# Optimization experiments

Hardware: AMD Instinct MI355X
Metric: run time of the kernel (lower is better)

## Reference

```python
import jax, jax.numpy as jnp
import numpy as np


def _lstm_cell(x, h, c, Wih, Whh, b):
    # torch LSTM gate order: i, f, g, o
    g = x @ Wih.T + h @ Whh.T + b
    i, f, gg, o = jnp.split(g, 4, axis=-1)
    c = jax.nn.sigmoid(f) * c + jax.nn.sigmoid(i) * jnp.tanh(gg)
    h = jax.nn.sigmoid(o) * jnp.tanh(c)
    return h, c


def _run_lstm(emb, mask, Wih, Whh, b, reverse):
    # mask-gated scan emulates pack_padded_sequence: state frozen on pad steps,
    # final (h, c) equals state at last valid token of each sequence.
    B = emb.shape[0]
    H = Whh.shape[1]
    def step(carry, inp):
        h, c = carry
        x, m = inp  # x: (B, E), m: (B, 1)
        hn, cn = _lstm_cell(x, h, c, Wih, Whh, b)
        h = m * hn + (1.0 - m) * h
        c = m * cn + (1.0 - m) * c
        return (h, c), h
    xs = (jnp.swapaxes(emb, 0, 1), jnp.swapaxes(mask, 0, 1)[..., None])
    z = jnp.zeros((B, H), emb.dtype)
    (h, c), outs = jax.lax.scan(step, (z, z), xs, reverse=reverse)
    return jnp.swapaxes(outs, 0, 1), h, c  # (B, T, H), (B, H), (B, H)


def setup_inputs() -> dict:
    key = jax.random.key(0)
    ks = iter(jax.random.split(key, 40))
    B, Te, Td, E, H, Ve, Vd = 32, 64, 32, 256, 512, 32000, 32000
    s = 0.05
    def rn(shape):
        return jax.random.normal(next(ks), shape, jnp.float32) * s
    def zz(n):
        return jnp.zeros((n,), jnp.float32)
    return {
        "enc_texts": jax.random.randint(next(ks), (B, Te), 0, Ve),
        "enc_mask": jnp.ones((B, Te), jnp.float32),
        "dec_texts": jax.random.randint(next(ks), (B, Td), 0, Vd),
        "enc_emb": rn((Ve, E)),
        "dec_emb": rn((Vd, E)),
        "Wih_f": rn((4 * H, E)), "Whh_f": rn((4 * H, H)), "b_f": zz(4 * H),
        "Wih_b": rn((4 * H, E)), "Whh_b": rn((4 * H, H)), "b_b": zz(4 * H),
        "Wih_d": rn((4 * H, E + 2 * H)), "Whh_d": rn((4 * H, H)), "b_d": zz(4 * H),
        "W_h": rn((H, 2 * H)), "b_h": zz(H),
        "W_c": rn((H, 2 * H)), "b_c": zz(H),
        "W_df": rn((2 * H, 2 * H)), "b_df": zz(2 * H),
        "W_ef": rn((2 * H, 2 * H)), "b_ef": zz(2 * H),
        "W_out": rn((Vd, 3 * H)), "b_out": zz(Vd),
    }


def reference(enc_texts, enc_mask, dec_texts, enc_emb, dec_emb,
              Wih_f, Whh_f, b_f, Wih_b, Whh_b, b_b,
              Wih_d, Whh_d, b_d, W_h, b_h, W_c, b_c,
              W_df, b_df, W_ef, b_ef, W_out, b_out):
    B = enc_texts.shape[0]
    H = Whh_d.shape[1]
    # ---- encode: bidirectional LSTM over embedded source ----
    emb = enc_emb[enc_texts]  # (B, Te, E)
    out_f, hf, cf = _run_lstm(emb, enc_mask, Wih_f, Whh_f, b_f, reverse=False)
    out_b, hb, cb = _run_lstm(emb, enc_mask, Wih_b, Whh_b, b_b, reverse=True)
    enc_output = jnp.concatenate([out_f, out_b], -1) * enc_mask[..., None]  # (B, Te, 2H)
    # ---- decode_init: project concat of directional final states ----
    dec_h = jax.nn.relu(jnp.concatenate([hf, hb], -1) @ W_h.T + b_h)  # (B, H)
    dec_c = jax.nn.relu(jnp.concatenate([cf, cb], -1) @ W_c.T + b_c)  # (B, H)
    # precompute attention keys once (enc_output_fc)
    enc_feat = enc_output @ W_ef.T + b_ef  # (B, Te, 2H)
    # teacher-forcing inputs: tokens 0..Td-2
    dec_in = dec_emb[dec_texts[:, :-1]]  # (B, Td-1, E)
    ctx0 = jnp.zeros((B, 2 * H), enc_output.dtype)

    def step(carry, x):
        h, c, ctx = carry
        xin = jnp.concatenate([x, ctx], -1)  # (B, E + 2H)
        h, c = _lstm_cell(xin, h, c, Wih_d, Whh_d, b_d)
        # dot attention: query from projected (h, c)
        df = jnp.concatenate([h, c], -1) @ W_df.T + b_df  # (B, 2H)
        scores = jnp.einsum('bd,btd->bt', df, enc_feat)
        a = jax.nn.softmax(scores, axis=-1) * enc_mask
        a = a / jnp.sum(a, axis=-1, keepdims=True)
        ctx = jnp.einsum('bt,btd->bd', a, enc_output)  # (B, 2H)
        logits = jnp.concatenate([h, ctx], -1) @ W_out.T + b_out  # (B, Vd)
        return (h, c, ctx), logits

    _, logits = jax.lax.scan(step, (dec_h, dec_c, ctx0), jnp.swapaxes(dec_in, 0, 1))
    return jnp.swapaxes(logits, 0, 1)  # (B, Td-1, Vd)
```

## Files before the change

### kernel.cpp

```cpp
#include <hip/hip_runtime.h>
#include <hip/hip_bf16.h>


typedef __attribute__((ext_vector_type(8))) short bfrag_t;
typedef __attribute__((ext_vector_type(4))) float f4_t;

static __device__ __forceinline__ float bf2f(unsigned short u) {
  union { float f; unsigned int i; } v; v.i = ((unsigned int)u) << 16; return v.f;
}
static __device__ __forceinline__ unsigned short f2bf(float f) {
  union { float f; unsigned int i; } v; v.f = f;
  unsigned int r = v.i + 0x7FFFu + ((v.i >> 16) & 1u);
  return (unsigned short)(r >> 16);
}
static __device__ __forceinline__ unsigned int pack_bf2(float lo, float hi) {
  __hip_bfloat162 h2 = __float22bfloat162_rn(make_float2(lo, hi));
  union { __hip_bfloat162 h; unsigned int u; } cv; cv.h = h2;
  return cv.u;
}
static __device__ __forceinline__ float sigm(float x) {
  return __builtin_amdgcn_rcpf(1.f + __expf(-x));
}
static __device__ __forceinline__ float ftanh(float x) {
  float e = __expf(2.f * x);
  return 1.f - 2.f * __builtin_amdgcn_rcpf(e + 1.f);
}

#define GLDS16(g, l)                                                        \
  __builtin_amdgcn_global_load_lds(                                         \
      (const __attribute__((address_space(1))) void*)(g),                   \
      (__attribute__((address_space(3))) void*)(l), 16, 0, 0)

static __device__ __forceinline__ void st_f32_coh(float* p, float v) {
  asm volatile("global_store_dword %0, %1, off sc0 sc1" :: "v"(p), "v"(v) : "memory");
}
static __device__ __forceinline__ void st_u16_coh(unsigned short* p, unsigned short x) {
  asm volatile("global_store_short %0, %1, off sc0 sc1" :: "v"(p), "v"((unsigned)x) : "memory");
}
static __device__ __forceinline__ float ld_f32_coh(const float* p) {
  float v;
  asm volatile("global_load_dword %0, %1, off sc0 sc1\n\ts_waitcnt vmcnt(0)"
               : "=v"(v) : "v"(p) : "memory");
  return v;
}

static __device__ __forceinline__ void gbar8(unsigned* base, unsigned target) {
  __syncthreads();
  if (threadIdx.x < 64) {
    if (threadIdx.x == 0)
      __hip_atomic_fetch_add(base + (blockIdx.x & 7) * 32, 1u,
                             __ATOMIC_RELAXED, __HIP_MEMORY_SCOPE_AGENT);
    unsigned sum;
    do {
      unsigned v = 0;
      if (threadIdx.x < 8)
        v = __hip_atomic_load(base + threadIdx.x * 32,
                              __ATOMIC_RELAXED, __HIP_MEMORY_SCOPE_AGENT);
      v += __shfl_xor(v, 1);
      v += __shfl_xor(v, 2);
      v += __shfl_xor(v, 4);
      sum = __shfl(v, 0);
      if (sum < target) __builtin_amdgcn_s_sleep(2);
    } while (sum < target);
  }
  __syncthreads();
}

__global__ __launch_bounds__(256) void gemm_bt_kernel(
    const unsigned short* __restrict__ A, int lda,
    const float* __restrict__ B, int ldb, int bcol0,
    const float* __restrict__ bias, void* __restrict__ Cv, int ldc,
    int Mvalid, int K, int Mt, int swz, int obf) {
  __shared__ unsigned short As[128 * 32];
  __shared__ unsigned short Bs[128 * 32];
  int id = blockIdx.x;
  if (swz) { int x = id & 7; id = x * ((int)gridDim.x >> 3) + (id >> 3); }
  const int mb = id % Mt, nb = id / Mt;
  const int m0 = mb * 128, n0 = nb * 128;
  const int tid = threadIdx.x;
  const int w = tid >> 6, lane = tid & 63;
  const int wr = (w >> 1) * 64, wc = (w & 1) * 64;
  const int l15 = lane & 15, l4 = lane >> 4;

  const int arow = w * 16 + (lane >> 2);
  const int acol = (lane & 3) * 8;
  const unsigned short* Ag = A + (size_t)(m0 + arow) * lda + acol;

  const int brow = tid >> 1;
  const int bcol = (tid & 1) * 16;
  const float* Bg = B + (size_t)(n0 + brow) * ldb + bcol0 + bcol;
  unsigned short* Bsw = Bs + brow * 32 + bcol;

  f4_t acc[4][4];
#pragma unroll
  for (int i = 0; i < 4; ++i)
#pragma unroll
    for (int j = 0; j < 4; ++j) {
      acc[i][j].x = 0.f; acc[i][j].y = 0.f; acc[i][j].z = 0.f; acc[i][j].w = 0.f;
    }

  for (int kt = 0; kt < K; kt += 32) {
    GLDS16(Ag + kt, As + w * 512);
    GLDS16(Ag + (size_t)64 * lda + kt, As + (4 + w) * 512);
    float4 q0 = *(const float4*)(Bg + kt);
    float4 q1 = *(const float4*)(Bg + kt + 4);
    float4 q2 = *(const float4*)(Bg + kt + 8);
    float4 q3 = *(const float4*)(Bg + kt + 12);
    union { unsigned int u[8]; uint4 q[2]; } pk;
    pk.u[0] = pack_bf2(q0.x, q0.y); pk.u[1] = pack_bf2(q0.z, q0.w);
    pk.u[2] = pack_bf2(q1.x, q1.y); pk.u[3] = pack_bf2(q1.z, q1.w);
    pk.u[4] = pack_bf2(q2.x, q2.y); pk.u[5] = pack_bf2(q2.z, q2.w);
    pk.u[6] = pack_bf2(q3.x, q3.y); pk.u[7] = pack_bf2(q3.z, q3.w);
    *(uint4*)(Bsw) = pk.q[0];
    *(uint4*)(Bsw + 8) = pk.q[1];
    __syncthreads();
    bfrag_t af[4], bfv[4];
#pragma unroll
    for (int m = 0; m < 4; ++m)
      af[m] = *(const bfrag_t*)(As + (wr + m * 16 + l15) * 32 + l4 * 8);
#pragma unroll
    for (int n = 0; n < 4; ++n)
      bfv[n] = *(const bfrag_t*)(Bs + (wc + n * 16 + l15) * 32 + l4 * 8);
#pragma unroll
    for (int m = 0; m < 4; ++m)
#pragma unroll
      for (int n = 0; n < 4; ++n)
        acc[m][n] = __builtin_amdgcn_mfma_f32_16x16x32_bf16(af[m], bfv[n], acc[m][n], 0, 0, 0);
    __syncthreads();
  }

  const int crb = l4 * 4;
  float* Cf = (float*)Cv;
  unsigned short* Ch = (unsigned short*)Cv;
#pragma unroll
  for (int m = 0; m < 4; ++m)
#pragma unroll
    for (int n = 0; n < 4; ++n)
#pragma unroll
      for (int r = 0; r < 4; ++r) {
        int gr = m0 + wr + m * 16 + crb + r;
        if (gr < Mvalid) {
          int gc = n0 + wc + n * 16 + l15;
          float v = acc[m][n][r] + (bias ? bias[gc] : 0.f);
          if (obf) Ch[(size_t)gr * ldc + gc] = f2bf(v);
          else     Cf[(size_t)gr * ldc + gc] = v;
        }
      }
}

__global__ void gather_enc_kernel(const int* __restrict__ texts,
                                  const float* __restrict__ table,
                                  unsigned short* __restrict__ out) {
  const int row = blockIdx.x;
  const int tok = texts[row];
  const float4 v = *(const float4*)(table + (size_t)tok * 256 + threadIdx.x * 4);
  unsigned short* o = out + (size_t)row * 256 + threadIdx.x * 4;
  o[0] = f2bf(v.x); o[1] = f2bf(v.y); o[2] = f2bf(v.z); o[3] = f2bf(v.w);
}

__global__ void gather_dec_kernel(const int* __restrict__ texts,
                                  const float* __restrict__ table,
                                  unsigned short* __restrict__ out) {
  const int row = blockIdx.x;
  unsigned short* o = out + (size_t)row * 256 + threadIdx.x * 4;
  if (row >= 992) { o[0] = 0; o[1] = 0; o[2] = 0; o[3] = 0; return; }
  const int b = row / 31, t2 = row - b * 31;
  const int tok = texts[b * 32 + t2];
  const float4 v = *(const float4*)(table + (size_t)tok * 256 + threadIdx.x * 4);
  o[0] = f2bf(v.x); o[1] = f2bf(v.y); o[2] = f2bf(v.z); o[3] = f2bf(v.w);
}

__global__ __launch_bounds__(256) void wdf_t_kernel(
    const float* __restrict__ W_df, const float* __restrict__ b_df,
    float* __restrict__ WT) {
  const int bid = blockIdx.x;
  if (bid < 1024) {
    __shared__ float tl[32][33];
    const int tx = (bid & 31) * 32, ty = (bid >> 5) * 32;
    const int r = threadIdx.x >> 5, c = threadIdx.x & 31;
#pragma unroll
    for (int i = 0; i < 4; ++i)
      tl[r + i * 8][c] = W_df[(size_t)(ty + r + i * 8) * 1024 + tx + c];
    __syncthreads();
#pragma unroll
    for (int i = 0; i < 4; ++i)
      WT[(size_t)(tx + r + i * 8) * 1024 + ty + c] = tl[c][r + i * 8];
  } else {
    for (int i = threadIdx.x; i < 1024; i += 256)
      WT[(size_t)1024 * 1024 + i] = b_df[i];
  }
}

__global__ __launch_bounds__(256) void mega_enc_kernel(
    const float* __restrict__ XF, const float* __restrict__ XB,
    const float* __restrict__ Whh_f, const float* __restrict__ Whh_b,
    const float* __restrict__ mask,
    unsigned short* __restrict__ HBF,
    unsigned short* __restrict__ ENCO, float* __restrict__ HFIN,
    unsigned* bar) {
  const int bi = blockIdx.x;
  const int dir = bi >> 7;
  const int u0 = (bi & 127) * 4;
  const int tid = threadIdx.x;
  const float* X = dir ? XB : XF;
  const float* W = dir ? Whh_b : Whh_f;
  unsigned short* Hbf = HBF + dir * 32768;
  unsigned* cnt = bar + dir * 256;

  __shared__ unsigned short WA[16 * 520];
  __shared__ unsigned short HB[32 * 520];
  __shared__ float Gl[16][33];

#pragma unroll
  for (int i = 0; i < 8; ++i) {
    int idx = tid + i * 256;
    int r = idx >> 7, c4 = idx & 127;
    const float4 v = *(const float4*)(W + (size_t)((r >> 2) * 512 + u0 + (r & 3)) * 512 + c4 * 4);
    *(uint2*)(WA + r * 520 + c4 * 4) = make_uint2(pack_bf2(v.x, v.y), pack_bf2(v.z, v.w));
  }
  __syncthreads();

  const int w = tid >> 6, lane = tid & 63;
  const int l15 = lane & 15, l4 = lane >> 4;

  bfrag_t afr[16];
  if (w < 2) {
#pragma unroll
    for (int kk = 0; kk < 16; ++kk)
      afr[kk] = *(const bfrag_t*)(WA + l15 * 520 + kk * 32 + l4 * 8);
  }

  const int ob = tid & 31, ouo = (tid >> 5) & 3;
  const int ou = u0 + ouo;
  float h_reg = 0.f, c_reg = 0.f;

  unsigned tgt = 0;
  for (int s = 0; s < 64; ++s) {
    const int t = dir ? (63 - s) : s;
    const int pp = s & 1;
    float xg0 = 0, xg1 = 0, xg2 = 0, xg3 = 0, mval = 0;
    if (tid < 128) {
      const float* xp = X + ((size_t)ob * 64 + t) * 2048 + ou;
      xg0 = xp[0]; xg1 = xp[512]; xg2 = xp[1024]; xg3 = xp[1536];
      mval = mask[ob * 64 + t];
    }
    const unsigned short* hsrc = Hbf + pp * 16384;
    uint4 tmp[8];
#pragma unroll
    for (int i = 0; i < 8; ++i) {
      int idx = tid + i * 256;
      int r = idx >> 6, c = idx & 63;
      asm volatile("global_load_dwordx4 %0, %1, off sc0 sc1"
                   : "=v"(tmp[i]) : "v"(hsrc + r * 512 + c * 8));
    }
    asm volatile("s_waitcnt vmcnt(0)" ::: "memory");
#pragma unroll
    for (int i = 0; i < 8; ++i) {
      int idx = tid + i * 256;
      int r = idx >> 6, c = idx & 63;
      *(uint4*)(HB + r * 520 + c * 8) = tmp[i];
    }
    __syncthreads();
    if (w < 2) {
      f4_t ae = {0.f, 0.f, 0.f, 0.f}, ao = {0.f, 0.f, 0.f, 0.f};
#pragma unroll
      for (int kk = 0; kk < 16; kk += 2) {
        bfrag_t b0 = *(const bfrag_t*)(HB + (w * 16 + l15) * 520 + kk * 32 + l4 * 8);
        bfrag_t b1 = *(const bfrag_t*)(HB + (w * 16 + l15) * 520 + (kk + 1) * 32 + l4 * 8);
        ae = __builtin_amdgcn_mfma_f32_16x16x32_bf16(afr[kk], b0, ae, 0, 0, 0);
        ao = __builtin_amdgcn_mfma_f32_16x16x32_bf16(afr[kk + 1], b1, ao, 0, 0, 0);
      }
#pragma unroll
      for (int r = 0; r < 4; ++r)
        Gl[l4 * 4 + r][w * 16 + l15] = ae[r] + ao[r];
    }
    __syncthreads();
    if (tid < 128) {
      float gi = Gl[ouo][ob] + xg0;
      float gf = Gl[4 + ouo][ob] + xg1;
      float gg = Gl[8 + ouo][ob] + xg2;
      float go = Gl[12 + ouo][ob] + xg3;
      float cn = sigm(gf) * c_reg + sigm(gi) * ftanh(gg);
      float hn = sigm(go) * ftanh(cn);
      float hmix = mval * hn + (1.f - mval) * h_reg;
      float cmix = mval * cn + (1.f - mval) * c_reg;
      h_reg = hmix; c_reg = cmix;
      ENCO[((size_t)ob * 64 + t) * 1024 + dir * 512 + ou] = f2bf(hmix * mval);
      st_u16_coh(Hbf + (pp ^ 1) * 16384 + ob * 512 + ou, f2bf(hmix));
      if (s == 63) {
        HFIN[dir * 16384 + ob * 512 + ou] = hmix;
        HFIN[(2 + dir) * 16384 + ob * 512 + ou] = cmix;
      }
    }
    if (s < 63) { tgt += 128; gbar8(cnt, tgt); }
  }
}

__global__ __launch_bounds__(256) void mega_dec_kernel(
    const float* __restrict__ HFIN, const float* __restrict__ W_h,
    const float* __restrict__ b_h, const float* __restrict__ W_c,
    const float* __restrict__ b_c, const float* __restrict__ XD,
    const float* __restrict__ Wih_d, const float* __restrict__ Whh_d,
    const unsigned short* __restrict__ EFG, const unsigned short* __restrict__ ENCO,
    const float* __restrict__ mask, float* __restrict__ DECH,
    float* __restrict__ DECC, unsigned short* __restrict__ PRE0,
    unsigned short* __restrict__ ACAT, unsigned* bar) {
  const int bi = blockIdx.x;
  const int tid = threadIdx.x;
  const bool is_attn = (bi >= 128);
  const int u0 = bi * 4;

  __shared__ union {
    struct {
      unsigned short wga[16 * 1544];
      unsigned short xb[32 * 1544];
      float gl[16][33];
    } s;
    struct {
      unsigned short efg[64 * 1160];
      float hcl[1024];
      float scl[64];
      float al[64];
    } a;
    struct { float xl[32][132]; float wi[8][132]; } ini;
  } U;

  if (!is_attn) {
    const int mat = bi >> 6, j0i = (bi & 63) * 8;
    const int jj = tid >> 5, b = tid & 31;
    const int sr = tid >> 5, sc = (tid & 31) * 4;
    const float* Wm = mat ? W_c : W_h;
    const float* bias = mat ? b_c : b_h;
    const float* x0 = HFIN + (size_t)(mat ? 2 : 0) * 16384;
    const float* x1 = HFIN + (size_t)(mat ? 3 : 1) * 16384;
    float acc = 0.f;
    for (int kc = 0; kc < 1024; kc += 128) {
#pragma unroll
      for (int i = 0; i < 4; ++i) {
        int r = sr + i * 8;
        const float* src = (kc < 512) ? (x0 + r * 512 + kc + sc)
                                      : (x1 + r * 512 + (kc - 512) + sc);
        *(float4*)&U.ini.xl[r][sc] = *(const float4*)src;
      }
      *(float4*)&U.ini.wi[sr][sc] = *(const float4*)(Wm + (size_t)(j0i + sr) * 1024 + kc + sc);
      __syncthreads();
#pragma unroll
      for (int k = 0; k < 128; k += 4) {
        float4 wv = *(const float4*)&U.ini.wi[jj][k];
        float4 xv = *(const float4*)&U.ini.xl[b][k];
        acc += wv.x * xv.x + wv.y * xv.y + wv.z * xv.z + wv.w * xv.w;
      }
      __syncthreads();
    }
    float v = fmaxf(acc + bias[j0i + jj], 0.f);
    if (mat == 0) {
      st_f32_coh(DECH + b * 512 + j0i + jj, v);
      st_u16_coh(PRE0 + (size_t)b * 1536 + j0i + jj, f2bf(v));
    } else {
      st_f32_coh(DECC + b * 512 + j0i + jj, v);
    }
  } else {
    const int b = bi - 128;
    for (int idx = tid; idx < 64 * 144; idx += 256) {
      int s = idx / 144, c16 = idx - (idx / 144) * 144;
      *(uint4*)(U.a.efg + s * 1160 + c16 * 8) =
          *(const uint4*)(EFG + ((size_t)b * 64 + s) * 1152 + c16 * 8);
    }
  }
  unsigned tgt = 160;
  gbar8(bar, tgt);

  const int ob = tid & 31, ouo = (tid >> 5) & 3, ou = u0 + ouo;
  const int w = tid >> 6, lane = tid & 63;
  const int l15 = lane & 15, l4 = lane >> 4;
  float h_reg = 0.f, c_reg = 0.f;

  if (!is_attn) {
#pragma unroll
    for (int i = 0; i < 24; ++i) {
      int idx = tid + i * 256;
      int r = idx / 384, c4 = idx - (idx / 384) * 384;
      int wrow = (r >> 2) * 512 + u0 + (r & 3);
      int c = c4 * 4;
      float4 v;
      if (c < 512) v = *(const float4*)(Whh_d + (size_t)wrow * 512 + c);
      else         v = *(const float4*)(Wih_d + (size_t)wrow * 1280 + 256 + (c - 512));
      *(uint2*)(U.s.wga + r * 1544 + c) = make_uint2(pack_bf2(v.x, v.y), pack_bf2(v.z, v.w));
    }
    if (tid < 128) {
      h_reg = ld_f32_coh(DECH + ob * 512 + ou);
      c_reg = ld_f32_coh(DECC + ob * 512 + ou);
    }
  }

  for (int t = 0; t < 31; ++t) {
    if (!is_attn) {
      float xg0 = 0, xg1 = 0, xg2 = 0, xg3 = 0;
      if (tid < 128) {
        const float* xp = XD + ((size_t)ob * 31 + t) * 2048 + ou;
        xg0 = xp[0]; xg1 = xp[512]; xg2 = xp[1024]; xg3 = xp[1536];
      }
      {
        uint4 tmp[24];
#pragma unroll
        for (int i = 0; i < 24; ++i) {
          int idx = tid + i * 256;
          int r = idx / 192, c16 = idx - (idx / 192) * 192;
          const unsigned short* src = (t == 0)
              ? (PRE0 + (size_t)r * 1536 + c16 * 8)
              : (ACAT + ((size_t)r * 31 + (t - 1)) * 1536 + c16 * 8);
          asm volatile("global_load_dwordx4 %0, %1, off sc0 sc1"
                       : "=v"(tmp[i]) : "v"(src));
        }
        asm volatile("s_waitcnt vmcnt(16)" ::: "memory");
#pragma unroll
        for (int i = 0; i < 8; ++i) {
          int idx = tid + i * 256;
          int r = idx / 192, c16 = idx - (idx / 192) * 192;
          *(uint4*)(U.s.xb + r * 1544 + c16 * 8) = tmp[i];
        }
        asm volatile("s_waitcnt vmcnt(8)" ::: "memory");
#pragma unroll
        for (int i = 8; i < 16; ++i) {
          int idx = tid + i * 256;
          int r = idx / 192, c16 = idx - (idx / 192) * 192;
          *(uint4*)(U.s.xb + r * 1544 + c16 * 8) = tmp[i];
        }
        asm volatile("s_waitcnt vmcnt(0)" ::: "memory");
#pragma unroll
        for (int i = 16; i < 24; ++i) {
          int idx = tid + i * 256;
          int r = idx / 192, c16 = idx - (idx / 192) * 192;
          *(uint4*)(U.s.xb + r * 1544 + c16 * 8) = tmp[i];
        }
      }
      __syncthreads();
      if (w < 2) {
        f4_t ae = {0.f, 0.f, 0.f, 0.f}, ao = {0.f, 0.f, 0.f, 0.f};
#pragma unroll
        for (int kk = 0; kk < 48; kk += 2) {
          bfrag_t a0 = *(const bfrag_t*)(U.s.wga + l15 * 1544 + kk * 32 + l4 * 8);
          bfrag_t b0 = *(const bfrag_t*)(U.s.xb + (w * 16 + l15) * 1544 + kk * 32 + l4 * 8);
          bfrag_t a1 = *(const bfrag_t*)(U.s.wga + l15 * 1544 + (kk + 1) * 32 + l4 * 8);
          bfrag_t b1 = *(const bfrag_t*)(U.s.xb + (w * 16 + l15) * 1544 + (kk + 1) * 32 + l4 * 8);
          ae = __builtin_amdgcn_mfma_f32_16x16x32_bf16(a0, b0, ae, 0, 0, 0);
          ao = __builtin_amdgcn_mfma_f32_16x16x32_bf16(a1, b1, ao, 0, 0, 0);
        }
#pragma unroll
        for (int r = 0; r < 4; ++r)
          U.s.gl[l4 * 4 + r][w * 16 + l15] = ae[r] + ao[r];
      }
      __syncthreads();
      if (tid < 128) {
        float gi = U.s.gl[ouo][ob] + xg0;
        float gf = U.s.gl[4 + ouo][ob] + xg1;
        float gg = U.s.gl[8 + ouo][ob] + xg2;
        float go = U.s.gl[12 + ouo][ob] + xg3;
        float cn = sigm(gf) * c_reg + sigm(gi) * ftanh(gg);
        float hn = sigm(go) * ftanh(cn);
        h_reg = hn; c_reg = cn;
        st_f32_coh(DECH + ob * 512 + ou, hn);
        st_f32_coh(DECC + ob * 512 + ou, cn);
        st_u16_coh(ACAT + ((size_t)ob * 31 + t) * 1536 + ou, f2bf(hn));
      }
    }
    tgt += 160;
    gbar8(bar, tgt);
    if (is_attn) {
      const int b = bi - 128;
      {
        int c = tid * 4;
        const float* hp = (c < 512) ? (DECH + b * 512 + c) : (DECC + b * 512 + (c - 512));
        uint4 hv;
        asm volatile("global_load_dwordx4 %0, %1, off sc0 sc1\n\ts_waitcnt vmcnt(0)"
                     : "=v"(hv) : "v"(hp) : "memory");
        *(uint4*)&U.a.hcl[c] = hv;
      }
      __syncthreads();
      {
        const int sidx = tid >> 2, part = tid & 3;
        const unsigned short* eg = U.a.efg + sidx * 1160 + part * 256;
        const float* d = &U.a.hcl[part * 256];
        float acc = 0.f;
#pragma unroll 8
        for (int k = 0; k < 256; k += 8) {
          uint4 v = *(const uint4*)(eg + k);
          acc += bf2f((unsigned short)(v.x & 0xFFFFu)) * d[k + 0];
          acc += bf2f((unsigned short)(v.x >> 16))     * d[k + 1];
          acc += bf2f((unsigned short)(v.y & 0xFFFFu)) * d[k + 2];
          acc += bf2f((unsigned short)(v.y >> 16))     * d[k + 3];
          acc += bf2f((unsigned short)(v.z & 0xFFFFu)) * d[k + 4];
          acc += bf2f((unsigned short)(v.z >> 16))     * d[k + 5];
          acc += bf2f((unsigned short)(v.w & 0xFFFFu)) * d[k + 6];
          acc += bf2f((unsigned short)(v.w >> 16))     * d[k + 7];
        }
        acc += __shfl_xor(acc, 1);
        acc += __shfl_xor(acc, 2);
        if (part == 0)
          U.a.scl[sidx] = acc + bf2f(U.a.efg[sidx * 1160 + 1024]);
      }
      __syncthreads();
      if (tid < 64) {
        float v = U.a.scl[tid];
        float mx = v;
#pragma unroll
        for (int o = 32; o >= 1; o >>= 1) mx = fmaxf(mx, __shfl_xor(mx, o));
        float e = __expf(v - mx) * mask[b * 64 + tid];
        float sm = e;
#pragma unroll
        for (int o = 32; o >= 1; o >>= 1) sm += __shfl_xor(sm, o);
        U.a.al[tid] = e / sm;
      }
      __syncthreads();
      float c0 = 0.f, c1 = 0.f, c2 = 0.f, c3 = 0.f;
#pragma unroll 8
      for (int tp = 0; tp < 64; ++tp) {
        float a = U.a.al[tp];
        const unsigned short* eo = ENCO + ((size_t)b * 64 + tp) * 1024 + tid;
        c0 += a * bf2f(eo[0]);
        c1 += a * bf2f(eo[256]);
        c2 += a * bf2f(eo[512]);
        c3 += a * bf2f(eo[768]);
      }
      unsigned short* ap = ACAT + ((size_t)b * 31 + t) * 1536 + 512;
      st_u16_coh(ap + tid, f2bf(c0));
      st_u16_coh(ap + tid + 256, f2bf(c1));
      st_u16_coh(ap + tid + 512, f2bf(c2));
      st_u16_coh(ap + tid + 768, f2bf(c3));
    }
    if (t < 30) { tgt += 160; gbar8(bar, tgt); }
  }
}

extern "C" void kernel_launch(void* const* d_in, const int* in_sizes, int n_in,
                              void* d_out, int out_size, void* d_ws, size_t ws_size,
                              hipStream_t stream) {
  const int*   enc_texts = (const int*)  d_in[0];
  const float* enc_mask  = (const float*)d_in[1];
  const int*   dec_texts = (const int*)  d_in[2];
  const float* enc_emb   = (const float*)d_in[3];
  const float* dec_emb   = (const float*)d_in[4];
  const float* Wih_f = (const float*)d_in[5];
  const float* Whh_f = (const float*)d_in[6];
  const float* b_f   = (const float*)d_in[7];
  const float* Wih_b = (const float*)d_in[8];
  const float* Whh_b = (const float*)d_in[9];
  const float* b_b   = (const float*)d_in[10];
  const float* Wih_d = (const float*)d_in[11];
  const float* Whh_d = (const float*)d_in[12];
  const float* b_d   = (const float*)d_in[13];
  const float* W_h   = (const float*)d_in[14];
  const float* b_h   = (const float*)d_in[15];
  const float* W_c   = (const float*)d_in[16];
  const float* b_c   = (const float*)d_in[17];
  const float* W_df  = (const float*)d_in[18];
  const float* b_df  = (const float*)d_in[19];
  const float* W_ef  = (const float*)d_in[20];
  const float* b_ef  = (const float*)d_in[21];
  const float* W_out = (const float*)d_in[22];
  const float* b_out = (const float*)d_in[23];
  float* out = (float*)d_out;

  char* ws = (char*)d_ws;
  size_t off = 0;
  auto alloc = [&](size_t bytes) {
    char* p = ws + off;
    off += (bytes + 255) & ~(size_t)255;
    return p;
  };
  unsigned short* HBF  = (unsigned short*)alloc((size_t)2 * 2 * 16384 * 2);
  float* DECH = (float*)alloc((size_t)16384 * 4);
  float* DECC = (float*)alloc((size_t)16384 * 4);
  unsigned short* PRE0 = (unsigned short*)alloc((size_t)32 * 1536 * 2);
  unsigned short* ACAT = (unsigned short*)alloc((size_t)1024 * 1536 * 2);
  unsigned* bar = (unsigned*)alloc(4096);
  size_t zbytes = off;
  float* XF = (float*)alloc((size_t)2048 * 2048 * 4);
  float* XB = (float*)alloc((size_t)2048 * 2048 * 4);
  float* XD = (float*)alloc((size_t)1024 * 2048 * 4);
  unsigned short* EFb  = (unsigned short*)alloc((size_t)2048 * 1024 * 2);
  unsigned short* ENCO = (unsigned short*)alloc((size_t)2048 * 1024 * 2);
  unsigned short* EMBB = (unsigned short*)alloc((size_t)2048 * 256 * 2);
  unsigned short* DEMB = (unsigned short*)alloc((size_t)1024 * 256 * 2);
  float* HFIN = (float*)alloc((size_t)4 * 16384 * 4);
  unsigned short* EFG = (unsigned short*)XF;
  float* WT  = XB;

  hipMemsetAsync(d_ws, 0, zbytes, stream);

  gather_enc_kernel<<<2048, 64, 0, stream>>>(enc_texts, enc_emb, EMBB);
  gather_dec_kernel<<<1024, 64, 0, stream>>>(dec_texts, dec_emb, DEMB);

  dim3 blk(256);
  gemm_bt_kernel<<<256, blk, 0, stream>>>(EMBB, 256, Wih_f, 256, 0, b_f, XF, 2048, 2048, 256, 16, 0, 0);
  gemm_bt_kernel<<<256, blk, 0, stream>>>(EMBB, 256, Wih_b, 256, 0, b_b, XB, 2048, 2048, 256, 16, 0, 0);
  gemm_bt_kernel<<<128, blk, 0, stream>>>(DEMB, 256, Wih_d, 1280, 0, b_d, XD, 2048, 1024, 256, 8, 0, 0);

  mega_enc_kernel<<<256, blk, 0, stream>>>(XF, XB, Whh_f, Whh_b, enc_mask, HBF, ENCO, HFIN, bar);

  wdf_t_kernel<<<1025, blk, 0, stream>>>(W_df, b_df, WT);
  gemm_bt_kernel<<<128, blk, 0, stream>>>(ENCO, 1024, W_ef, 1024, 0, b_ef, EFb, 1024, 2048, 1024, 16, 0, 1);
  gemm_bt_kernel<<<144, blk, 0, stream>>>(EFb, 1024, WT, 1024, 0, nullptr, EFG, 1152, 2048, 1024, 16, 0, 1);

  mega_dec_kernel<<<160, blk, 0, stream>>>(HFIN, W_h, b_h, W_c, b_c, XD, Wih_d, Whh_d,
                                           EFG, ENCO, enc_mask, DECH, DECC, PRE0, ACAT, bar + 512);

  gemm_bt_kernel<<<2000, blk, 0, stream>>>(ACAT, 1536, W_out, 1536, 0, b_out, out, 32000, 992, 1536, 8, 1, 0);
}
```

Baseline: 1.346 ms.

## Halve encoder blocks and split decoder barrier into two overlapped phases

The encoder recurrence now uses 128 blocks that each own 8 hidden units, with all four waves doing MFMA work. This halves the number of blocks taking part in each per-step grid barrier. In the decoder, the single 160-block barrier becomes two split arrive/wait barriers, one between LSTM blocks and one from attention blocks to LSTM blocks. The LSTM blocks precompute the h-part of the next step's gate GEMM while the attention context is still being computed, which shortens the serial critical path per step. The cost is more complex synchronization, with a risk of ordering or coherence bugs, and higher per-block work and register use in the encoder.

```diff
diff --git a/kernel.cpp b/kernel.cpp
--- a/kernel.cpp
+++ b/kernel.cpp
@@ -44,12 +44,14 @@
   return v;
 }
 
-static __device__ __forceinline__ void gbar8(unsigned* base, unsigned target) {
+static __device__ __forceinline__ void arrive8(unsigned* base) {
   __syncthreads();
+  if (threadIdx.x == 0)
+    __hip_atomic_fetch_add(base + (blockIdx.x & 7) * 32, 1u,
+                           __ATOMIC_RELAXED, __HIP_MEMORY_SCOPE_AGENT);
+}
+static __device__ __forceinline__ void wait8(unsigned* base, unsigned target) {
   if (threadIdx.x < 64) {
-    if (threadIdx.x == 0)
-      __hip_atomic_fetch_add(base + (blockIdx.x & 7) * 32, 1u,
-                             __ATOMIC_RELAXED, __HIP_MEMORY_SCOPE_AGENT);
     unsigned sum;
     do {
       unsigned v = 0;
@@ -64,6 +66,10 @@
     } while (sum < target);
   }
   __syncthreads();
+}
+static __device__ __forceinline__ void gbar8(unsigned* base, unsigned target) {
+  arrive8(base);
+  wait8(base, target);
 }
 
 __global__ __launch_bounds__(256) void gemm_bt_kernel(
@@ -199,38 +205,37 @@
     unsigned short* __restrict__ ENCO, float* __restrict__ HFIN,
     unsigned* bar) {
   const int bi = blockIdx.x;
-  const int dir = bi >> 7;
-  const int u0 = (bi & 127) * 4;
+  const int dir = bi >> 6;
+  const int u0 = (bi & 63) * 8;
   const int tid = threadIdx.x;
   const float* X = dir ? XB : XF;
   const float* W = dir ? Whh_b : Whh_f;
   unsigned short* Hbf = HBF + dir * 32768;
   unsigned* cnt = bar + dir * 256;
 
-  __shared__ unsigned short WA[16 * 520];
+  __shared__ unsigned short WA[32 * 520];
   __shared__ unsigned short HB[32 * 520];
-  __shared__ float Gl[16][33];
-
-#pragma unroll
-  for (int i = 0; i < 8; ++i) {
+  __shared__ float Gl[32][33];
+
+#pragma unroll
+  for (int i = 0; i < 16; ++i) {
     int idx = tid + i * 256;
     int r = idx >> 7, c4 = idx & 127;
-    const float4 v = *(const float4*)(W + (size_t)((r >> 2) * 512 + u0 + (r & 3)) * 512 + c4 * 4);
+    const float4 v = *(const float4*)(W + (size_t)((r >> 3) * 512 + u0 + (r & 7)) * 512 + c4 * 4);
     *(uint2*)(WA + r * 520 + c4 * 4) = make_uint2(pack_bf2(v.x, v.y), pack_bf2(v.z, v.w));
   }
   __syncthreads();
 
   const int w = tid >> 6, lane = tid & 63;
   const int l15 = lane & 15, l4 = lane >> 4;
+  const int wrow = (w >> 1) * 16, wcol = (w & 1) * 16;
 
   bfrag_t afr[16];
-  if (w < 2) {
-#pragma unroll
-    for (int kk = 0; kk < 16; ++kk)
-      afr[kk] = *(const bfrag_t*)(WA + l15 * 520 + kk * 32 + l4 * 8);
-  }
-
-  const int ob = tid & 31, ouo = (tid >> 5) & 3;
+#pragma unroll
+  for (int kk = 0; kk < 16; ++kk)
+    afr[kk] = *(const bfrag_t*)(WA + (wrow + l15) * 520 + kk * 32 + l4 * 8);
+
+  const int ob = tid & 31, ouo = tid >> 5;
   const int ou = u0 + ouo;
   float h_reg = 0.f, c_reg = 0.f;
 
@@ -238,12 +243,9 @@
   for (int s = 0; s < 64; ++s) {
     const int t = dir ? (63 - s) : s;
     const int pp = s & 1;
-    float xg0 = 0, xg1 = 0, xg2 = 0, xg3 = 0, mval = 0;
-    if (tid < 128) {
-      const float* xp = X + ((size_t)ob * 64 + t) * 2048 + ou;
-      xg0 = xp[0]; xg1 = xp[512]; xg2 = xp[1024]; xg3 = xp[1536];
-      mval = mask[ob * 64 + t];
-    }
+    const float* xp = X + ((size_t)ob * 64 + t) * 2048 + ou;
+    float xg0 = xp[0], xg1 = xp[512], xg2 = xp[1024], xg3 = xp[1536];
+    float mval = mask[ob * 64 + t];
     const unsigned short* hsrc = Hbf + pp * 16384;
     uint4 tmp[8];
 #pragma unroll
@@ -261,25 +263,25 @@
       *(uint4*)(HB + r * 520 + c * 8) = tmp[i];
     }
     __syncthreads();
-    if (w < 2) {
+    {
       f4_t ae = {0.f, 0.f, 0.f, 0.f}, ao = {0.f, 0.f, 0.f, 0.f};
 #pragma unroll
       for (int kk = 0; kk < 16; kk += 2) {
-        bfrag_t b0 = *(const bfrag_t*)(HB + (w * 16 + l15) * 520 + kk * 32 + l4 * 8);
-        bfrag_t b1 = *(const bfrag_t*)(HB + (w * 16 + l15) * 520 + (kk + 1) * 32 + l4 * 8);
+        bfrag_t b0 = *(const bfrag_t*)(HB + (wcol + l15) * 520 + kk * 32 + l4 * 8);
+        bfrag_t b1 = *(const bfrag_t*)(HB + (wcol + l15) * 520 + (kk + 1) * 32 + l4 * 8);
         ae = __builtin_amdgcn_mfma_f32_16x16x32_bf16(afr[kk], b0, ae, 0, 0, 0);
         ao = __builtin_amdgcn_mfma_f32_16x16x32_bf16(afr[kk + 1], b1, ao, 0, 0, 0);
       }
 #pragma unroll
       for (int r = 0; r < 4; ++r)
-        Gl[l4 * 4 + r][w * 16 + l15] = ae[r] + ao[r];
+        Gl[wrow + l4 * 4 + r][wcol + l15] = ae[r] + ao[r];
     }
     __syncthreads();
-    if (tid < 128) {
+    {
       float gi = Gl[ouo][ob] + xg0;
-      float gf = Gl[4 + ouo][ob] + xg1;
-      float gg = Gl[8 + ouo][ob] + xg2;
-      float go = Gl[12 + ouo][ob] + xg3;
+      float gf = Gl[8 + ouo][ob] + xg1;
+      float gg = Gl[16 + ouo][ob] + xg2;
+      float go = Gl[24 + ouo][ob] + xg3;
       float cn = sigm(gf) * c_reg + sigm(gi) * ftanh(gg);
       float hn = sigm(go) * ftanh(cn);
       float hmix = mval * hn + (1.f - mval) * h_reg;
@@ -292,7 +294,7 @@
         HFIN[(2 + dir) * 16384 + ob * 512 + ou] = cmix;
       }
     }
-    if (s < 63) { tgt += 128; gbar8(cnt, tgt); }
+    if (s < 63) { tgt += 64; gbar8(cnt, tgt); }
   }
 }
 
@@ -309,6 +311,8 @@
   const int tid = threadIdx.x;
   const bool is_attn = (bi >= 128);
   const int u0 = bi * 4;
+  unsigned* barB1 = bar;
+  unsigned* barB2 = bar + 256;
 
   __shared__ union {
     struct {
@@ -325,57 +329,49 @@
     struct { float xl[32][132]; float wi[8][132]; } ini;
   } U;
 
-  if (!is_attn) {
-    const int mat = bi >> 6, j0i = (bi & 63) * 8;
-    const int jj = tid >> 5, b = tid & 31;
-    const int sr = tid >> 5, sc = (tid & 31) * 4;
-    const float* Wm = mat ? W_c : W_h;
-    const float* bias = mat ? b_c : b_h;
-    const float* x0 = HFIN + (size_t)(mat ? 2 : 0) * 16384;
-    const float* x1 = HFIN + (size_t)(mat ? 3 : 1) * 16384;
-    float acc = 0.f;
-    for (int kc = 0; kc < 1024; kc += 128) {
-#pragma unroll
-      for (int i = 0; i < 4; ++i) {
-        int r = sr + i * 8;
-        const float* src = (kc < 512) ? (x0 + r * 512 + kc + sc)
-                                      : (x1 + r * 512 + (kc - 512) + sc);
-        *(float4*)&U.ini.xl[r][sc] = *(const float4*)src;
-      }
-      *(float4*)&U.ini.wi[sr][sc] = *(const float4*)(Wm + (size_t)(j0i + sr) * 1024 + kc + sc);
-      __syncthreads();
-#pragma unroll
-      for (int k = 0; k < 128; k += 4) {
-        float4 wv = *(const float4*)&U.ini.wi[jj][k];
-        float4 xv = *(const float4*)&U.ini.xl[b][k];
-        acc += wv.x * xv.x + wv.y * xv.y + wv.z * xv.z + wv.w * xv.w;
-      }
-      __syncthreads();
-    }
-    float v = fmaxf(acc + bias[j0i + jj], 0.f);
-    if (mat == 0) {
-      st_f32_coh(DECH + b * 512 + j0i + jj, v);
-      st_u16_coh(PRE0 + (size_t)b * 1536 + j0i + jj, f2bf(v));
-    } else {
-      st_f32_coh(DECC + b * 512 + j0i + jj, v);
-    }
-  } else {
-    const int b = bi - 128;
-    for (int idx = tid; idx < 64 * 144; idx += 256) {
-      int s = idx / 144, c16 = idx - (idx / 144) * 144;
-      *(uint4*)(U.a.efg + s * 1160 + c16 * 8) =
-          *(const uint4*)(EFG + ((size_t)b * 64 + s) * 1152 + c16 * 8);
-    }
-  }
-  unsigned tgt = 160;
-  gbar8(bar, tgt);
-
   const int ob = tid & 31, ouo = (tid >> 5) & 3, ou = u0 + ouo;
   const int w = tid >> 6, lane = tid & 63;
   const int l15 = lane & 15, l4 = lane >> 4;
-  float h_reg = 0.f, c_reg = 0.f;
 
   if (!is_attn) {
+    {
+      const int mat = bi >> 6, j0i = (bi & 63) * 8;
+      const int jj = tid >> 5, b = tid & 31;
+      const int sr = tid >> 5, sc = (tid & 31) * 4;
+      const float* Wm = mat ? W_c : W_h;
+      const float* bias = mat ? b_c : b_h;
+      const float* x0 = HFIN + (size_t)(mat ? 2 : 0) * 16384;
+      const float* x1 = HFIN + (size_t)(mat ? 3 : 1) * 16384;
+      float acc = 0.f;
+      for (int kc = 0; kc < 1024; kc += 128) {
+#pragma unroll
+        for (int i = 0; i < 4; ++i) {
+          int r = sr + i * 8;
+          const float* src = (kc < 512) ? (x0 + r * 512 + kc + sc)
+                                        : (x1 + r * 512 + (kc - 512) + sc);
+          *(float4*)&U.ini.xl[r][sc] = *(const float4*)src;
+        }
+        *(float4*)&U.ini.wi[sr][sc] = *(const float4*)(Wm + (size_t)(j0i + sr) * 1024 + kc + sc);
+        __syncthreads();
+#pragma unroll
+        for (int k = 0; k < 128; k += 4) {
+          float4 wv = *(const float4*)&U.ini.wi[jj][k];
+          float4 xv = *(const float4*)&U.ini.xl[b][k];
+          acc += wv.x * xv.x + wv.y * xv.y + wv.z * xv.z + wv.w * xv.w;
+        }
+        __syncthreads();
+      }
+      float v = fmaxf(acc + bias[j0i + jj], 0.f);
+      if (mat == 0) {
+        st_f32_coh(DECH + b * 512 + j0i + jj, v);
+        st_u16_coh(PRE0 + (size_t)b * 1536 + j0i + jj, f2bf(v));
+      } else {
+        st_f32_coh(DECC + b * 512 + j0i + jj, v);
+      }
+    }
+    arrive8(barB1);
+    wait8(barB1, 128);
+
 #pragma unroll
     for (int i = 0; i < 24; ++i) {
       int idx = tid + i * 256;
@@ -387,68 +383,92 @@
       else         v = *(const float4*)(Wih_d + (size_t)wrow * 1280 + 256 + (c - 512));
       *(uint2*)(U.s.wga + r * 1544 + c) = make_uint2(pack_bf2(v.x, v.y), pack_bf2(v.z, v.w));
     }
+    float h_reg = 0.f, c_reg = 0.f;
     if (tid < 128) {
       h_reg = ld_f32_coh(DECH + ob * 512 + ou);
       c_reg = ld_f32_coh(DECC + ob * 512 + ou);
     }
-  }
-
-  for (int t = 0; t < 31; ++t) {
-    if (!is_attn) {
+
+    f4_t cae = {0.f, 0.f, 0.f, 0.f}, cao = {0.f, 0.f, 0.f, 0.f};
+
+    for (int t = 0; t < 31; ++t) {
       float xg0 = 0, xg1 = 0, xg2 = 0, xg3 = 0;
       if (tid < 128) {
         const float* xp = XD + ((size_t)ob * 31 + t) * 2048 + ou;
         xg0 = xp[0]; xg1 = xp[512]; xg2 = xp[1024]; xg3 = xp[1536];
       }
-      {
+      if (t == 0) {
         uint4 tmp[24];
 #pragma unroll
         for (int i = 0; i < 24; ++i) {
           int idx = tid + i * 256;
           int r = idx / 192, c16 = idx - (idx / 192) * 192;
-          const unsigned short* src = (t == 0)
-              ? (PRE0 + (size_t)r * 1536 + c16 * 8)
-              : (ACAT + ((size_t)r * 31 + (t - 1)) * 1536 + c16 * 8);
           asm volatile("global_load_dwordx4 %0, %1, off sc0 sc1"
-                       : "=v"(tmp[i]) : "v"(src));
-        }
-        asm volatile("s_waitcnt vmcnt(16)" ::: "memory");
-#pragma unroll
-        for (int i = 0; i < 8; ++i) {
+                       : "=v"(tmp[i]) : "v"(PRE0 + (size_t)r * 1536 + c16 * 8));
+        }
+        asm volatile("s_waitcnt vmcnt(0)" ::: "memory");
+#pragma unroll
+        for (int i = 0; i < 24; ++i) {
           int idx = tid + i * 256;
           int r = idx / 192, c16 = idx - (idx / 192) * 192;
           *(uint4*)(U.s.xb + r * 1544 + c16 * 8) = tmp[i];
         }
+        __syncthreads();
+        if (w < 2) {
+          f4_t ae = {0.f, 0.f, 0.f, 0.f}, ao = {0.f, 0.f, 0.f, 0.f};
+#pragma unroll
+          for (int kk = 0; kk < 48; kk += 2) {
+            bfrag_t a0 = *(const bfrag_t*)(U.s.wga + l15 * 1544 + kk * 32 + l4 * 8);
+            bfrag_t b0 = *(const bfrag_t*)(U.s.xb + (w * 16 + l15) * 1544 + kk * 32 + l4 * 8);
+            bfrag_t a1 = *(const bfrag_t*)(U.s.wga + l15 * 1544 + (kk + 1) * 32 + l4 * 8);
+            bfrag_t b1 = *(const bfrag_t*)(U.s.xb + (w * 16 + l15) * 1544 + (kk + 1) * 32 + l4 * 8);
+            ae = __builtin_amdgcn_mfma_f32_16x16x32_bf16(a0, b0, ae, 0, 0, 0);
+            ao = __builtin_amdgcn_mfma_f32_16x16x32_bf16(a1, b1, ao, 0, 0, 0);
+          }
+#pragma unroll
+          for (int r = 0; r < 4; ++r)
+            U.s.gl[l4 * 4 + r][w * 16 + l15] = ae[r] + ao[r];
+        }
+      } else {
+        wait8(barB2, 32u * t);
+        uint4 tmp[16];
+#pragma unroll
+        for (int i = 0; i < 16; ++i) {
+          int idx = tid + i * 256;
+          int r = idx >> 7, c16 = 64 + (idx & 127);
+          asm volatile("global_load_dwordx4 %0, %1, off sc0 sc1"
+                       : "=v"(tmp[i]) : "v"(ACAT + ((size_t)r * 31 + (t - 1)) * 1536 + c16 * 8));
+        }
         asm volatile("s_waitcnt vmcnt(8)" ::: "memory");
+#pragma unroll
+        for (int i = 0; i < 8; ++i) {
+          int idx = tid + i * 256;
+          int r = idx >> 7, c16 = 64 + (idx & 127);
+          *(uint4*)(U.s.xb + r * 1544 + c16 * 8) = tmp[i];
+        }
+        asm volatile("s_waitcnt vmcnt(0)" ::: "memory");
 #pragma unroll
         for (int i = 8; i < 16; ++i) {
           int idx = tid + i * 256;
-          int r = idx / 192, c16 = idx - (idx / 192) * 192;
+          int r = idx >> 7, c16 = 64 + (idx & 127);
           *(uint4*)(U.s.xb + r * 1544 + c16 * 8) = tmp[i];
         }
-        asm volatile("s_waitcnt vmcnt(0)" ::: "memory");
-#pragma unroll
-        for (int i = 16; i < 24; ++i) {
-          int idx = tid + i * 256;
-          int r = idx / 192, c16 = idx - (idx / 192) * 192;
-          *(uint4*)(U.s.xb + r * 1544 + c16 * 8) = tmp[i];
-        }
-      }
-      __syncthreads();
-      if (w < 2) {
-        f4_t ae = {0.f, 0.f, 0.f, 0.f}, ao = {0.f, 0.f, 0.f, 0.f};
-#pragma unroll
-        for (int kk = 0; kk < 48; kk += 2) {
-          bfrag_t a0 = *(const bfrag_t*)(U.s.wga + l15 * 1544 + kk * 32 + l4 * 8);
-          bfrag_t b0 = *(const bfrag_t*)(U.s.xb + (w * 16 + l15) * 1544 + kk * 32 + l4 * 8);
-          bfrag_t a1 = *(const bfrag_t*)(U.s.wga + l15 * 1544 + (kk + 1) * 32 + l4 * 8);
-          bfrag_t b1 = *(const bfrag_t*)(U.s.xb + (w * 16 + l15) * 1544 + (kk + 1) * 32 + l4 * 8);
-          ae = __builtin_amdgcn_mfma_f32_16x16x32_bf16(a0, b0, ae, 0, 0, 0);
-          ao = __builtin_amdgcn_mfma_f32_16x16x32_bf16(a1, b1, ao, 0, 0, 0);
-        }
-#pragma unroll
-        for (int r = 0; r < 4; ++r)
-          U.s.gl[l4 * 4 + r][w * 16 + l15] = ae[r] + ao[r];
+        __syncthreads();
+        if (w < 2) {
+          f4_t ae = cae, ao = cao;
+#pragma unroll
+          for (int kk = 16; kk < 48; kk += 2) {
+            bfrag_t a0 = *(const bfrag_t*)(U.s.wga + l15 * 1544 + kk * 32 + l4 * 8);
+            bfrag_t b0 = *(const bfrag_t*)(U.s.xb + (w * 16 + l15) * 1544 + kk * 32 + l4 * 8);
+            bfrag_t a1 = *(const bfrag_t*)(U.s.wga + l15 * 1544 + (kk + 1) * 32 + l4 * 8);
+            bfrag_t b1 = *(const bfrag_t*)(U.s.xb + (w * 16 + l15) * 1544 + (kk + 1) * 32 + l4 * 8);
+            ae = __builtin_amdgcn_mfma_f32_16x16x32_bf16(a0, b0, ae, 0, 0, 0);
+            ao = __builtin_amdgcn_mfma_f32_16x16x32_bf16(a1, b1, ao, 0, 0, 0);
+          }
+#pragma unroll
+          for (int r = 0; r < 4; ++r)
+            U.s.gl[l4 * 4 + r][w * 16 + l15] = ae[r] + ao[r];
+        }
       }
       __syncthreads();
       if (tid < 128) {
@@ -463,11 +483,49 @@
         st_f32_coh(DECC + ob * 512 + ou, cn);
         st_u16_coh(ACAT + ((size_t)ob * 31 + t) * 1536 + ou, f2bf(hn));
       }
-    }
-    tgt += 160;
-    gbar8(bar, tgt);
-    if (is_attn) {
-      const int b = bi - 128;
+      arrive8(barB1);
+      if (t < 30) {
+        wait8(barB1, 128u * (t + 2));
+        uint4 pre[8];
+#pragma unroll
+        for (int i = 0; i < 8; ++i) {
+          int idx = tid + i * 256;
+          int r = idx >> 6, c16 = idx & 63;
+          asm volatile("global_load_dwordx4 %0, %1, off sc0 sc1"
+                       : "=v"(pre[i]) : "v"(ACAT + ((size_t)r * 31 + t) * 1536 + c16 * 8));
+        }
+        asm volatile("s_waitcnt vmcnt(0)" ::: "memory");
+#pragma unroll
+        for (int i = 0; i < 8; ++i) {
+          int idx = tid + i * 256;
+          int r = idx >> 6, c16 = idx & 63;
+          *(uint4*)(U.s.xb + r * 1544 + c16 * 8) = pre[i];
+        }
+        __syncthreads();
+        if (w < 2) {
+          f4_t ae = {0.f, 0.f, 0.f, 0.f}, ao = {0.f, 0.f, 0.f, 0.f};
+#pragma unroll
+          for (int kk = 0; kk < 16; kk += 2) {
+            bfrag_t a0 = *(const bfrag_t*)(U.s.wga + l15 * 1544 + kk * 32 + l4 * 8);
+            bfrag_t b0 = *(const bfrag_t*)(U.s.xb + (w * 16 + l15) * 1544 + kk * 32 + l4 * 8);
+            bfrag_t a1 = *(const bfrag_t*)(U.s.wga + l15 * 1544 + (kk + 1) * 32 + l4 * 8);
+            bfrag_t b1 = *(const bfrag_t*)(U.s.xb + (w * 16 + l15) * 1544 + (kk + 1) * 32 + l4 * 8);
+            ae = __builtin_amdgcn_mfma_f32_16x16x32_bf16(a0, b0, ae, 0, 0, 0);
+            ao = __builtin_amdgcn_mfma_f32_16x16x32_bf16(a1, b1, ao, 0, 0, 0);
+          }
+          cae = ae; cao = ao;
+        }
+      }
+    }
+  } else {
+    const int b = bi - 128;
+    for (int idx = tid; idx < 64 * 144; idx += 256) {
+      int s = idx / 144, c16 = idx - (idx / 144) * 144;
+      *(uint4*)(U.a.efg + s * 1160 + c16 * 8) =
+          *(const uint4*)(EFG + ((size_t)b * 64 + s) * 1152 + c16 * 8);
+    }
+    for (int t = 0; t < 31; ++t) {
+      wait8(barB1, 128u * (t + 2));
       {
         int c = tid * 4;
         const float* hp = (c < 512) ? (DECH + b * 512 + c) : (DECC + b * 512 + (c - 512));
@@ -527,8 +585,8 @@
       st_u16_coh(ap + tid + 256, f2bf(c1));
       st_u16_coh(ap + tid + 512, f2bf(c2));
       st_u16_coh(ap + tid + 768, f2bf(c3));
-    }
-    if (t < 30) { tgt += 160; gbar8(bar, tgt); }
+      arrive8(barB2);
+    }
   }
 }
 
@@ -574,6 +632,7 @@
   unsigned short* PRE0 = (unsigned short*)alloc((size_t)32 * 1536 * 2);
   unsigned short* ACAT = (unsigned short*)alloc((size_t)1024 * 1536 * 2);
   unsigned* bar = (unsigned*)alloc(4096);
+  unsigned* barD = bar + 512;
   size_t zbytes = off;
   float* XF = (float*)alloc((size_t)2048 * 2048 * 4);
   float* XB = (float*)alloc((size_t)2048 * 2048 * 4);
@@ -596,14 +655,14 @@
   gemm_bt_kernel<<<256, blk, 0, stream>>>(EMBB, 256, Wih_b, 256, 0, b_b, XB, 2048, 2048, 256, 16, 0, 0);
   gemm_bt_kernel<<<128, blk, 0, stream>>>(DEMB, 256, Wih_d, 1280, 0, b_d, XD, 2048, 1024, 256, 8, 0, 0);
 
-  mega_enc_kernel<<<256, blk, 0, stream>>>(XF, XB, Whh_f, Whh_b, enc_mask, HBF, ENCO, HFIN, bar);
+  mega_enc_kernel<<<128, blk, 0, stream>>>(XF, XB, Whh_f, Whh_b, enc_mask, HBF, ENCO, HFIN, bar);
 
   wdf_t_kernel<<<1025, blk, 0, stream>>>(W_df, b_df, WT);
   gemm_bt_kernel<<<128, blk, 0, stream>>>(ENCO, 1024, W_ef, 1024, 0, b_ef, EFb, 1024, 2048, 1024, 16, 0, 1);
   gemm_bt_kernel<<<144, blk, 0, stream>>>(EFb, 1024, WT, 1024, 0, nullptr, EFG, 1152, 2048, 1024, 16, 0, 1);
 
   mega_dec_kernel<<<160, blk, 0, stream>>>(HFIN, W_h, b_h, W_c, b_c, XD, Wih_d, Whh_d,
-                                           EFG, ENCO, enc_mask, DECH, DECC, PRE0, ACAT, bar + 512);
+                                           EFG, ENCO, enc_mask, DECH, DECC, PRE0, ACAT, barD);
 
   gemm_bt_kernel<<<2000, blk, 0, stream>>>(ACAT, 1536, W_out, 1536, 0, b_out, out, 32000, 992, 1536, 8, 1, 0);
 }
```

Result: faster. 1.248 ms (-7.3%).
